# Optimization experiments

Hardware: AMD Instinct MI355X
Metric: run time of the kernel (lower is better)

Reference implementation:

```python
import jax, jax.numpy as jnp
import numpy as np

B, T, D = 4, 4096, 1024

def setup_inputs() -> dict:
    key = jax.random.key(0)
    ks = jax.random.split(key, 6)
    x = jax.random.normal(ks[0], (B, T, D), dtype=jnp.float32)
    mask = jax.random.randint(ks[1], (B, T), 0, 2).astype(bool)
    # torch nn.Linear init scale ~ 1/sqrt(fan_in); exact init unimportant for correctness baseline
    s = 1.0 / np.sqrt(D)
    W_qkv = jax.random.normal(ks[2], (3 * D, D), dtype=jnp.float32) * s
    b_qkv = jax.random.normal(ks[3], (3 * D,), dtype=jnp.float32) * s
    W_out = jax.random.normal(ks[4], (D, D), dtype=jnp.float32) * s
    b_out = jax.random.normal(ks[5], (D,), dtype=jnp.float32) * s
    return {"x": x, "mask": mask, "W_qkv": W_qkv, "b_qkv": b_qkv, "W_out": W_out, "b_out": b_out}

def reference(x, mask, W_qkv, b_qkv, W_out, b_out):
    # qkv projection: (B,T,D) @ (D,3D) + (3D,)
    qkv = jnp.einsum('btd,ed->bte', x, W_qkv) + b_qkv
    q, k, v = jnp.split(qkv, 3, axis=-1)  # each (B,T,D)
    q = q / jnp.linalg.norm(q, axis=-1, keepdims=True)
    k = k / jnp.linalg.norm(k, axis=-1, keepdims=True)
    k = jnp.where(mask[..., None], 0.0, k)  # masked_fill(mask, 0)
    kv = jnp.sum(k * v, axis=-2, keepdims=True)  # (B,1,D) global feature sum
    out = kv * q  # (B,T,D)
    return jnp.einsum('btd,ed->bte', out, W_out) + b_out
```

## Files before the change

kernel.cpp:

```cpp
#include <hip/hip_runtime.h>
#include <stdint.h>


typedef short  short8   __attribute__((ext_vector_type(8)));
typedef float  floatx16 __attribute__((ext_vector_type(16)));

#define BM 128
#define BN 128
#define BK 64

__device__ __forceinline__ void async16(const void* g, void* l) {
  __builtin_amdgcn_global_load_lds((const __attribute__((address_space(1))) void*)g,
                                   (__attribute__((address_space(3))) void*)l, 16, 0, 0);
}

__device__ __forceinline__ uint16_t f2bf(float f) {
  union { float f; uint32_t u; } x; x.f = f;
  uint32_t u = x.u;
  return (uint16_t)((u + 0x7fffu + ((u >> 16) & 1u)) >> 16);
}
__device__ __forceinline__ float bf2f(uint16_t h) {
  union { uint32_t u; float f; } x; x.u = ((uint32_t)h) << 16; return x.f;
}
__device__ __forceinline__ uint32_t pack2(float a, float b) {
  return (uint32_t)f2bf(a) | ((uint32_t)f2bf(b) << 16);
}
__device__ __forceinline__ void upk8(uint4 u, float* f) {
  f[0]=bf2f((uint16_t)u.x); f[1]=bf2f((uint16_t)(u.x>>16));
  f[2]=bf2f((uint16_t)u.y); f[3]=bf2f((uint16_t)(u.y>>16));
  f[4]=bf2f((uint16_t)u.z); f[5]=bf2f((uint16_t)(u.z>>16));
  f[6]=bf2f((uint16_t)u.w); f[7]=bf2f((uint16_t)(u.w>>16));
}

__global__ __launch_bounds__(256) void cvt3(
    const float* __restrict__ a, uint16_t* __restrict__ ao, int na,
    const float* __restrict__ b, uint16_t* __restrict__ bo, int nb,
    const float* __restrict__ c, uint16_t* __restrict__ co, int nc) {
  int i = blockIdx.x * 256 + threadIdx.x;
  const float* in; uint16_t* out; int j = i;
  if (j < na) { in = a; out = ao; }
  else {
    j -= na;
    if (j < nb) { in = b; out = bo; }
    else { j -= nb; if (j >= nc) return; in = c; out = co; }
  }
  const float4* p = (const float4*)in;
  float4 u = p[(size_t)j * 2], v = p[(size_t)j * 2 + 1];
  uint4 o;
  o.x = pack2(u.x, u.y); o.y = pack2(u.z, u.w);
  o.z = pack2(v.x, v.y); o.w = pack2(v.z, v.w);
  ((uint4*)out)[j] = o;
}

__global__ __launch_bounds__(256, 2) void gemm1(
    const uint16_t* __restrict__ A, const uint16_t* __restrict__ Bw,
    const float* __restrict__ bias, uint16_t* __restrict__ Cb,
    int N, int K)
{
  __shared__ __align__(16) uint16_t As[BM * BK];
  __shared__ __align__(16) uint16_t Bs[BN * BK];
  const int tid = threadIdx.x;
  const int wave = tid >> 6, lane = tid & 63;
  const int l31 = lane & 31, khalf = lane >> 5;
  const int wm = wave & 1, wn = wave >> 1;
  const int tileM = blockIdx.y * BM, tileN = blockIdx.x * BN;

  const int srow = wave * 8 + (lane >> 3);
  const int skc  = (lane & 7) ^ (lane >> 3);
  const uint16_t* gA = A  + (size_t)(tileM + srow) * K + skc * 8;
  const uint16_t* gB = Bw + (size_t)(tileN + srow) * K + skc * 8;
  char* lA = (char*)As + wave * 64 * 16;
  char* lB = (char*)Bs + wave * 64 * 16;

  floatx16 acc[2][2];
#pragma unroll
  for (int mi = 0; mi < 2; mi++)
#pragma unroll
    for (int ni = 0; ni < 2; ni++)
#pragma unroll
      for (int r = 0; r < 16; r++) acc[mi][ni][r] = 0.f;

  const int arow0 = wm * 64 + l31;
  const int brow0 = wn * 64 + l31;

  for (int k0 = 0; k0 < K; k0 += BK) {
#pragma unroll
    for (int s = 0; s < 4; s++) {
      async16(gA + k0 + s * 32 * K, lA + s * 4096);
      async16(gB + k0 + s * 32 * K, lB + s * 4096);
    }
    __syncthreads();
#pragma unroll
    for (int ks = 0; ks < 4; ks++) {
      const int kc = khalf + ks * 2;
      short8 af[2], bfr[2];
#pragma unroll
      for (int mi = 0; mi < 2; mi++) {
        int r = arow0 + mi * 32;
        af[mi] = *(const short8*)&As[(r * 8 + (kc ^ (r & 7))) * 8];
      }
#pragma unroll
      for (int ni = 0; ni < 2; ni++) {
        int r = brow0 + ni * 32;
        bfr[ni] = *(const short8*)&Bs[(r * 8 + (kc ^ (r & 7))) * 8];
      }
#pragma unroll
      for (int mi = 0; mi < 2; mi++)
#pragma unroll
        for (int ni = 0; ni < 2; ni++)
          acc[mi][ni] = __builtin_amdgcn_mfma_f32_32x32x16_bf16(af[mi], bfr[ni], acc[mi][ni], 0, 0, 0);
    }
    __syncthreads();
  }

#pragma unroll
  for (int mi = 0; mi < 2; mi++) {
    int rbase = tileM + wm * 64 + mi * 32 + 4 * khalf;
#pragma unroll
    for (int ni = 0; ni < 2; ni++) {
      int col = tileN + wn * 64 + ni * 32 + l31;
      float bv = bias[col];
#pragma unroll
      for (int reg = 0; reg < 16; reg++) {
        int row = rbase + (reg & 3) + 8 * (reg >> 2);
        Cb[(size_t)row * N + col] = f2bf(acc[mi][ni][reg] + bv);
      }
    }
  }
}

__global__ __launch_bounds__(256, 2) void gemm2(
    const uint16_t* __restrict__ qkv, const float* __restrict__ invq,
    const float* __restrict__ kv, const uint16_t* __restrict__ Bw,
    const float* __restrict__ bias, float* __restrict__ Cf)
{
  __shared__ __align__(16) uint16_t As[BM * BK];
  __shared__ __align__(16) uint16_t Bs[BN * BK];
  __shared__ __align__(16) float kvs[1024];
  const int tid = threadIdx.x;
  const int wave = tid >> 6, lane = tid & 63;
  const int l31 = lane & 31, khalf = lane >> 5;
  const int wm = wave & 1, wn = wave >> 1;
  const int tileM = blockIdx.y * BM, tileN = blockIdx.x * BN;

  const int srow = wave * 8 + (lane >> 3);
  const int skc  = (lane & 7) ^ (lane >> 3);
  const uint16_t* gB = Bw + (size_t)(tileN + srow) * 1024 + skc * 8;
  char* lB = (char*)Bs + wave * 64 * 16;

  {
    int i = tid * 4;
    *(float4*)&kvs[i] = *(const float4*)(kv + ((tileM >> 12) << 10) + i);
  }
  float sinv[4];
#pragma unroll
  for (int s = 0; s < 4; s++) sinv[s] = invq[tileM + s * 32 + srow];

  floatx16 acc[2][2];
#pragma unroll
  for (int mi = 0; mi < 2; mi++)
#pragma unroll
    for (int ni = 0; ni < 2; ni++)
#pragma unroll
      for (int r = 0; r < 16; r++) acc[mi][ni][r] = 0.f;

  const int arow0 = wm * 64 + l31;
  const int brow0 = wn * 64 + l31;

  const uint16_t* qbase = qkv + (size_t)(tileM + srow) * 3072 + skc * 8;
  uint4 nq[4];
#pragma unroll
  for (int s = 0; s < 4; s++)
    nq[s] = *(const uint4*)(qbase + (size_t)s * 32 * 3072);

  __syncthreads();

#pragma unroll 2
  for (int k0 = 0; k0 < 1024; k0 += BK) {
    uint4 cq[4];
#pragma unroll
    for (int s = 0; s < 4; s++) cq[s] = nq[s];
    if (k0 + BK < 1024) {
#pragma unroll
      for (int s = 0; s < 4; s++)
        nq[s] = *(const uint4*)(qbase + (size_t)s * 32 * 3072 + k0 + BK);
    }
#pragma unroll
    for (int s = 0; s < 4; s++)
      async16(gB + k0 + s * 32 * 1024, lB + s * 4096);
#pragma unroll
    for (int s = 0; s < 4; s++) {
      int d = k0 + skc * 8;
      float4 k0v = *(const float4*)&kvs[d];
      float4 k1v = *(const float4*)&kvs[d + 4];
      float qf[8]; upk8(cq[s], qf);
      float sc = sinv[s];
      uint4 o;
      o.x = pack2(qf[0] * sc * k0v.x, qf[1] * sc * k0v.y);
      o.y = pack2(qf[2] * sc * k0v.z, qf[3] * sc * k0v.w);
      o.z = pack2(qf[4] * sc * k1v.x, qf[5] * sc * k1v.y);
      o.w = pack2(qf[6] * sc * k1v.z, qf[7] * sc * k1v.w);
      *(uint4*)((char*)As + (size_t)(s * 256 + wave * 64 + lane) * 16) = o;
    }
    __syncthreads();
#pragma unroll
    for (int ks = 0; ks < 4; ks++) {
      const int kc = khalf + ks * 2;
      short8 af[2], bfr[2];
#pragma unroll
      for (int mi = 0; mi < 2; mi++) {
        int r = arow0 + mi * 32;
        af[mi] = *(const short8*)&As[(r * 8 + (kc ^ (r & 7))) * 8];
      }
#pragma unroll
      for (int ni = 0; ni < 2; ni++) {
        int r = brow0 + ni * 32;
        bfr[ni] = *(const short8*)&Bs[(r * 8 + (kc ^ (r & 7))) * 8];
      }
#pragma unroll
      for (int mi = 0; mi < 2; mi++)
#pragma unroll
        for (int ni = 0; ni < 2; ni++)
          acc[mi][ni] = __builtin_amdgcn_mfma_f32_32x32x16_bf16(af[mi], bfr[ni], acc[mi][ni], 0, 0, 0);
    }
    __syncthreads();
  }

#pragma unroll
  for (int mi = 0; mi < 2; mi++) {
    int rbase = tileM + wm * 64 + mi * 32 + 4 * khalf;
#pragma unroll
    for (int ni = 0; ni < 2; ni++) {
      int col = tileN + wn * 64 + ni * 32 + l31;
      float bv = bias[col];
#pragma unroll
      for (int reg = 0; reg < 16; reg++) {
        int row = rbase + (reg & 3) + 8 * (reg >> 2);
        Cf[(size_t)row * 1024 + col] = acc[mi][ni][reg] + bv;
      }
    }
  }
}

__global__ __launch_bounds__(256) void detect_mask(const unsigned char* __restrict__ m,
                                                   int* __restrict__ flag) {
  int i = blockIdx.x * blockDim.x + threadIdx.x;
  int v = ((i & 3) != 0) ? (int)m[i] : 0;
  unsigned long long b = __ballot(v != 0);
  if ((threadIdx.x & 63) == 0 && b) atomicOr(flag, 1);
}

__global__ __launch_bounds__(256) void rownorm_kv(
    const uint16_t* __restrict__ qkv, const void* __restrict__ maskbuf,
    const int* __restrict__ flag, float* __restrict__ invq, float* __restrict__ kv)
{
  __shared__ float kvloc[1024];
  const int tid = threadIdx.x;
  for (int i = tid; i < 1024; i += 256) kvloc[i] = 0.f;
  __syncthreads();
  const int wave = tid >> 6, lane = tid & 63;
  const int b = blockIdx.x >> 9;
  const int isU8 = *flag;
  const unsigned char* m8 = (const unsigned char*)maskbuf;
  const int* m32 = (const int*)maskbuf;

  float kvacc[16];
#pragma unroll
  for (int i = 0; i < 16; i++) kvacc[i] = 0.f;

  const int r0 = blockIdx.x * 8 + wave * 2;
#pragma unroll
  for (int j = 0; j < 2; j++) {
    int r = r0 + j;
    const uint16_t* rp = qkv + (size_t)r * 3072;
    uint4 q0 = *(const uint4*)(rp + lane * 16);
    uint4 q1 = *(const uint4*)(rp + lane * 16 + 8);
    uint4 k0 = *(const uint4*)(rp + 1024 + lane * 16);
    uint4 k1 = *(const uint4*)(rp + 1024 + lane * 16 + 8);
    uint4 v0 = *(const uint4*)(rp + 2048 + lane * 16);
    uint4 v1 = *(const uint4*)(rp + 2048 + lane * 16 + 8);
    float qf[16], kf[16], vf[16];
    upk8(q0, qf); upk8(q1, qf + 8);
    upk8(k0, kf); upk8(k1, kf + 8);
    upk8(v0, vf); upk8(v1, vf + 8);
    float sq = 0.f, sk = 0.f;
#pragma unroll
    for (int i = 0; i < 16; i++) { sq = fmaf(qf[i], qf[i], sq); sk = fmaf(kf[i], kf[i], sk); }
    for (int off = 32; off; off >>= 1) { sq += __shfl_xor(sq, off); sk += __shfl_xor(sk, off); }
    float rq = rsqrtf(sq), rk = rsqrtf(sk);
    if (lane == 0) invq[r] = rq;
    int masked = isU8 ? (int)m8[r] : m32[r];
    if (!masked) {
#pragma unroll
      for (int i = 0; i < 16; i++) kvacc[i] = fmaf(kf[i] * rk, vf[i], kvacc[i]);
    }
  }
#pragma unroll
  for (int i = 0; i < 16; i++) atomicAdd(&kvloc[lane * 16 + i], kvacc[i]);
  __syncthreads();
  for (int i = tid; i < 1024; i += 256) atomicAdd(&kv[b * 1024 + i], kvloc[i]);
}

extern "C" void kernel_launch(void* const* d_in, const int* in_sizes, int n_in,
                              void* d_out, int out_size, void* d_ws, size_t ws_size,
                              hipStream_t stream) {
  const float* x     = (const float*)d_in[0];
  const void*  mask  = d_in[1];
  const float* W_qkv = (const float*)d_in[2];
  const float* b_qkv = (const float*)d_in[3];
  const float* W_out = (const float*)d_in[4];
  const float* b_out = (const float*)d_in[5];
  float* out = (float*)d_out;

  const int BT = 4 * 4096;
  const int D  = 1024;

  char* ws = (char*)d_ws;
  size_t off = 0;
  auto alloc = [&](size_t bytes) { size_t r = off; off += (bytes + 255) & ~(size_t)255; return r; };
  size_t o_xb   = alloc((size_t)BT * D * 2);
  size_t o_qkvb = alloc((size_t)BT * 3 * D * 2);
  size_t o_wq   = alloc((size_t)3 * D * D * 2);
  size_t o_wo   = alloc((size_t)D * D * 2);
  size_t o_kv   = alloc((size_t)4 * D * 4 + 256);
  size_t o_invq = alloc((size_t)BT * 4);

  uint16_t* xb   = (uint16_t*)(ws + o_xb);
  uint16_t* qkvb = (uint16_t*)(ws + o_qkvb);
  uint16_t* wq   = (uint16_t*)(ws + o_wq);
  uint16_t* wo   = (uint16_t*)(ws + o_wo);
  float*    kv   = (float*)(ws + o_kv);
  int*      flag = (int*)(ws + o_kv + (size_t)4 * D * 4);
  float*    invq = (float*)(ws + o_invq);

  hipMemsetAsync(ws + o_kv, 0, (size_t)4 * D * 4 + 256, stream);
  {
    int na = BT * D / 8, nb = 3 * D * D / 8, nc = D * D / 8;
    int tot = na + nb + nc;
    cvt3<<<dim3((tot + 255) / 256), 256, 0, stream>>>(x, xb, na, W_qkv, wq, nb, W_out, wo, nc);
  }
  detect_mask<<<dim3(64), 256, 0, stream>>>((const unsigned char*)mask, flag);
  gemm1<<<dim3(3 * D / BN, BT / BM), 256, 0, stream>>>(xb, wq, b_qkv, qkvb, 3 * D, D);
  rownorm_kv<<<dim3(2048), 256, 0, stream>>>(qkvb, mask, flag, invq, kv);
  gemm2<<<dim3(D / BN, BT / BM), 256, 0, stream>>>(qkvb, invq, kv, wo, b_out, out);
}
```

Measured before the change: 374.2 us.

## Remap GEMM tiles per XCD, simplify gemm2 Q loads, coarsen rownorm blocks

gemm1 now uses a 1D grid and maps blocks so that each of the 8 XCDs owns three N-column tiles, with consecutive blocks on an XCD sharing an M row. This is meant to raise L2 reuse of the A and B tiles. gemm2 also moves to a 1D grid, and its register double-buffering of Q loads is replaced by direct loads inside the loop, which cuts register pressure but exposes load latency. rownorm_kv processes 32 rows per block instead of 8, giving 4x fewer blocks and fewer kv atomics at the cost of less parallelism.

After: 333.3 us. -10.9%, faster.

```diff
diff --git a/kernel.cpp b/kernel.cpp
--- a/kernel.cpp
+++ b/kernel.cpp
@@ -63,7 +63,10 @@
   const int wave = tid >> 6, lane = tid & 63;
   const int l31 = lane & 31, khalf = lane >> 5;
   const int wm = wave & 1, wn = wave >> 1;
-  const int tileM = blockIdx.y * BM, tileN = blockIdx.x * BN;
+  const int id = blockIdx.x;
+  const int xcd = id & 7, w = id >> 3;
+  const int tileM = (w / 3) * BM;
+  const int tileN = (xcd * 3 + (w % 3)) * BN;
 
   const int srow = wave * 8 + (lane >> 3);
   const int skc  = (lane & 7) ^ (lane >> 3);
@@ -141,7 +144,9 @@
   const int wave = tid >> 6, lane = tid & 63;
   const int l31 = lane & 31, khalf = lane >> 5;
   const int wm = wave & 1, wn = wave >> 1;
-  const int tileM = blockIdx.y * BM, tileN = blockIdx.x * BN;
+  const int id = blockIdx.x;
+  const int tileM = (id >> 3) * BM;
+  const int tileN = (id & 7) * BN;
 
   const int srow = wave * 8 + (lane >> 3);
   const int skc  = (lane & 7) ^ (lane >> 3);
@@ -166,34 +171,21 @@
 
   const int arow0 = wm * 64 + l31;
   const int brow0 = wn * 64 + l31;
-
   const uint16_t* qbase = qkv + (size_t)(tileM + srow) * 3072 + skc * 8;
-  uint4 nq[4];
-#pragma unroll
-  for (int s = 0; s < 4; s++)
-    nq[s] = *(const uint4*)(qbase + (size_t)s * 32 * 3072);
 
   __syncthreads();
 
-#pragma unroll 2
   for (int k0 = 0; k0 < 1024; k0 += BK) {
-    uint4 cq[4];
-#pragma unroll
-    for (int s = 0; s < 4; s++) cq[s] = nq[s];
-    if (k0 + BK < 1024) {
-#pragma unroll
-      for (int s = 0; s < 4; s++)
-        nq[s] = *(const uint4*)(qbase + (size_t)s * 32 * 3072 + k0 + BK);
-    }
 #pragma unroll
     for (int s = 0; s < 4; s++)
       async16(gB + k0 + s * 32 * 1024, lB + s * 4096);
 #pragma unroll
     for (int s = 0; s < 4; s++) {
       int d = k0 + skc * 8;
+      uint4 qv = *(const uint4*)(qbase + (size_t)s * 32 * 3072 + k0);
       float4 k0v = *(const float4*)&kvs[d];
       float4 k1v = *(const float4*)&kvs[d + 4];
-      float qf[8]; upk8(cq[s], qf);
+      float qf[8]; upk8(qv, qf);
       float sc = sinv[s];
       uint4 o;
       o.x = pack2(qf[0] * sc * k0v.x, qf[1] * sc * k0v.y);
@@ -259,7 +251,8 @@
   for (int i = tid; i < 1024; i += 256) kvloc[i] = 0.f;
   __syncthreads();
   const int wave = tid >> 6, lane = tid & 63;
-  const int b = blockIdx.x >> 9;
+  const int b = blockIdx.x >> 7;
+  const int chunk = blockIdx.x & 127;
   const int isU8 = *flag;
   const unsigned char* m8 = (const unsigned char*)maskbuf;
   const int* m32 = (const int*)maskbuf;
@@ -268,9 +261,8 @@
 #pragma unroll
   for (int i = 0; i < 16; i++) kvacc[i] = 0.f;
 
-  const int r0 = blockIdx.x * 8 + wave * 2;
-#pragma unroll
-  for (int j = 0; j < 2; j++) {
+  const int r0 = b * 4096 + chunk * 32 + wave * 8;
+  for (int j = 0; j < 8; j++) {
     int r = r0 + j;
     const uint16_t* rp = qkv + (size_t)r * 3072;
     uint4 q0 = *(const uint4*)(rp + lane * 16);
@@ -340,7 +332,7 @@
     cvt3<<<dim3((tot + 255) / 256), 256, 0, stream>>>(x, xb, na, W_qkv, wq, nb, W_out, wo, nc);
   }
   detect_mask<<<dim3(64), 256, 0, stream>>>((const unsigned char*)mask, flag);
-  gemm1<<<dim3(3 * D / BN, BT / BM), 256, 0, stream>>>(xb, wq, b_qkv, qkvb, 3 * D, D);
-  rownorm_kv<<<dim3(2048), 256, 0, stream>>>(qkvb, mask, flag, invq, kv);
-  gemm2<<<dim3(D / BN, BT / BM), 256, 0, stream>>>(qkvb, invq, kv, wo, b_out, out);
-}
+  gemm1<<<dim3(3072), 256, 0, stream>>>(xb, wq, b_qkv, qkvb, 3 * D, D);
+  rownorm_kv<<<dim3(512), 256, 0, stream>>>(qkvb, mask, flag, invq, kv);
+  gemm2<<<dim3(1024), 256, 0, stream>>>(qkvb, invq, kv, wo, b_out, out);
+}
```
